# Kernel optimization log

Hardware: AMD Instinct MI355X
Metric: run time of the kernel (lower is better)

## Reference

```python
import jax, jax.numpy as jnp
import numpy as np
from jax import lax

HEADS = 8
DIM_HEAD = 64
MODALITIES = 8
QUERY_DIM = 128
INNER = HEADS * DIM_HEAD  # 512


def _conv(x, w):
    # x: (b, Cin, H, W), w: (Cout, Cin, kh, kw), VALID padding (padding done manually)
    return lax.conv_general_dilated(x, w, window_strides=(1, 1), padding='VALID',
                                    dimension_numbers=('NCHW', 'OIHW', 'NCHW'))


def _reflect_pad_w(x):
    # ReflectionPad2d((2,2,0,0)): pad width (last) axis by 2 on each side
    return jnp.pad(x, ((0, 0), (0, 0), (0, 0), (2, 2)), mode='reflect')


def setup_inputs() -> dict:
    key = jax.random.key(0)
    k1, k2, k3, k4 = jax.random.split(key, 4)
    b, n, m, c = 2, 4096, MODALITIES, QUERY_DIM
    x = jax.random.normal(k1, (b, n, m, c), dtype=jnp.float32)
    Wq = jax.random.normal(k2, (INNER, c, 1, 5), dtype=jnp.float32) * 0.02
    Wkv = jax.random.normal(k3, (2 * INNER, c, 1, 5), dtype=jnp.float32) * 0.02
    Wout = jax.random.normal(k4, (c * m, INNER, m, 5), dtype=jnp.float32) * 0.02
    return {"x": x, "Wq": Wq, "Wkv": Wkv, "Wout": Wout}


def reference(x, Wq, Wkv, Wout):
    b, n, m, c = x.shape
    h, d = HEADS, DIM_HEAD
    scale = d ** -0.5

    xp = _reflect_pad_w(jnp.transpose(x, (0, 3, 2, 1)))  # (b, c, m, n+4)
    q = _conv(xp, Wq)                                     # (b, h*d, m, n)
    kv = _conv(xp, Wkv)                                   # (b, 2*h*d, m, n)
    k, v = kv[:, :h * d], kv[:, h * d:]

    # channel axis (h d) split: h outer, d inner -> (b, h, d, m, n)
    q = q.reshape(b, h, d, m, n)
    k = k.reshape(b, h, d, m, n)
    v = v.reshape(b, h, d, m, n)

    # attention over sequence axis n; feature dim is (m d) per head
    sim = jnp.einsum('bhdmi,bhdmj->bhij', q, k) * scale   # (b, h, n, n)
    attn = jax.nn.softmax(sim, axis=-1)
    out = jnp.einsum('bhij,bhdmj->bhdmi', attn, v)        # (b, h, d, m, n)

    out = out.reshape(b, h * d, m, n)                     # 'b (h d) m n'
    o = _conv(_reflect_pad_w(out), Wout)                  # (b, c*m, 1, n)
    o = o.reshape(b, c, m, 1, n)[:, :, :, 0, :]           # squeeze height-1 dim -> (b, c, m, n)
    return o.reshape(x.shape)                             # torch .view(x_shape) is a raw reshape
```

## Files before the change

### kernel.cpp

```cpp
#include <hip/hip_runtime.h>
#include <stdint.h>


typedef __attribute__((ext_vector_type(8))) short short8;
typedef __attribute__((ext_vector_type(4))) short short4v;
typedef __attribute__((ext_vector_type(2))) short short2v;
typedef __attribute__((ext_vector_type(4))) float f32x4;
typedef __attribute__((ext_vector_type(16))) float f32x16;

__device__ __forceinline__ f32x4 mfma16(short8 a, short8 b, f32x4 c) {
  return __builtin_amdgcn_mfma_f32_16x16x32_bf16(a, b, c, 0, 0, 0);
}
__device__ __forceinline__ f32x16 mfma32(short8 a, short8 b, f32x16 c) {
  return __builtin_amdgcn_mfma_f32_32x32x16_bf16(a, b, c, 0, 0, 0);
}

__device__ __forceinline__ unsigned short f2bf(float f) {
  union { float f; uint32_t u; } v; v.f = f;
  uint32_t r = (v.u + 0x7fffu + ((v.u >> 16) & 1u)) >> 16;
  return (unsigned short)r;
}

__device__ __forceinline__ uint32_t cvtpk(float lo, float hi) {
  uint32_t r;
  asm volatile("v_cvt_pk_bf16_f32 %0, %1, %2" : "=v"(r) : "v"(lo), "v"(hi));
  return r;
}
__device__ __forceinline__ void plswap(uint32_t& a, uint32_t& b) {
  asm volatile("v_permlane32_swap_b32 %0, %1" : "+v"(a), "+v"(b));
}

__device__ __forceinline__ int refl4096(int p) {
  p = p < 0 ? -p : p;
  return p >= 4096 ? 8190 - p : p;
}

__device__ __forceinline__ void gl_lds16(const void* g, void* l) {
  __builtin_amdgcn_global_load_lds(
      (const __attribute__((address_space(1))) void*)g,
      (__attribute__((address_space(3))) void*)l, 16, 0, 0);
}

__global__ void k_convw_qkv(const float* __restrict__ Wq,
                            const float* __restrict__ Wkv,
                            unsigned short* __restrict__ out) {
  int e = blockIdx.x * 256 + threadIdx.x;
  int oc = e / 640, k = e - oc * 640;
  int ci = k & 127, t = k >> 7;
  float w = (oc < 512) ? Wq[oc * 640 + ci * 5 + t]
                       : Wkv[(oc - 512) * 640 + ci * 5 + t];
  out[e] = f2bf(w);
}

__global__ __launch_bounds__(256)
void k_convx(const float* __restrict__ x, unsigned short* __restrict__ xb,
             int b) {
  int e = (blockIdx.x * 256 + threadIdx.x) * 8;
  const float* src = x + (size_t)b * 4194304 + e;
  f32x4 v0 = *(const f32x4*)src;
  f32x4 v1 = *(const f32x4*)(src + 4);
  short8 pk;
  pk[0] = (short)f2bf(v0[0]); pk[1] = (short)f2bf(v0[1]);
  pk[2] = (short)f2bf(v0[2]); pk[3] = (short)f2bf(v0[3]);
  pk[4] = (short)f2bf(v1[0]); pk[5] = (short)f2bf(v1[1]);
  pk[6] = (short)f2bf(v1[2]); pk[7] = (short)f2bf(v1[3]);
  *(short8*)(xb + e) = pk;
}

__global__ __launch_bounds__(256)
void k_convw_out(const float* __restrict__ Wout,
                 unsigned short* __restrict__ out) {
  __shared__ unsigned short row_l[20480];
  const int oc = blockIdx.x;
  const int tid = threadIdx.x;
  const float* src = Wout + (size_t)oc * 20480;
#pragma unroll
  for (int i0 = 0; i0 < 5120; i0 += 256) {
    int i = i0 + tid;
    f32x4 v = *(const f32x4*)(src + (size_t)i * 4);
    short4v pk;
    pk[0] = (short)f2bf(v[0]); pk[1] = (short)f2bf(v[1]);
    pk[2] = (short)f2bf(v[2]); pk[3] = (short)f2bf(v[3]);
    *(short4v*)(row_l + i * 4) = pk;
  }
  __syncthreads();
  unsigned short* drow = out + (size_t)oc * 20480;
#pragma unroll
  for (int r0 = 0; r0 < 20480; r0 += 512) {
    int e = r0 + tid * 2;
    int t0 = e >> 12, ft0 = e & 4095;
    int t1 = (e + 1) >> 12, ft1 = (e + 1) & 4095;
    short2v pk;
    pk[0] = (short)row_l[(ft0 >> 3) * 40 + (ft0 & 7) * 5 + t0];
    pk[1] = (short)row_l[(ft1 >> 3) * 40 + (ft1 & 7) * 5 + t1];
    *(short2v*)(drow + e) = pk;
  }
}

__global__ __launch_bounds__(256)
void k_reduce(const float* __restrict__ P, float* __restrict__ outp, int b) {
  int e = (blockIdx.x * 256 + threadIdx.x) * 4;
  f32x4 a = *(const f32x4*)(P + e);
  f32x4 c = *(const f32x4*)(P + 4194304 + e);
  f32x4 s = (f32x4){a[0] + c[0], a[1] + c[1], a[2] + c[2], a[3] + c[3]};
  *(f32x4*)(outp + (size_t)b * 4194304 + e) = s;
}

__global__ __launch_bounds__(256, 2)
void k_qkv(const unsigned short* __restrict__ xb,
           const unsigned short* __restrict__ Wb,
           unsigned short* __restrict__ Qg, unsigned short* __restrict__ Kg,
           unsigned short* __restrict__ Vg) {
  __shared__ __align__(16) unsigned short As[2][8192];
  __shared__ __align__(16) unsigned short Bs[2][8192];
  const int tid = threadIdx.x;
  const int lane = tid & 63, w = tid >> 6;
  const int wr = w >> 1, wc = w & 1;
  const int l15 = lane & 15, lg = lane >> 4;
  const int p0 = blockIdx.x * 128;
  const int ocb = blockIdx.y * 128;
  const int m = blockIdx.z;

  f32x4 acc[4][4];
#pragma unroll
  for (int i = 0; i < 4; i++)
#pragma unroll
    for (int j = 0; j < 4; j++) acc[i][j] = (f32x4){0.f, 0.f, 0.f, 0.f};

  auto stage = [&](int ks, int d) {
    const int t = ks >> 1;
    const int ci0 = (ks & 1) << 6;
#pragma unroll
    for (int i = 0; i < 4; i++) {
      int s = tid + (i << 8);
      int row = s >> 3, c = s & 7;
      int cs = c ^ (row & 7);
      int xn = refl4096(p0 + row - 2 + t);
      gl_lds16(xb + (((size_t)xn << 3) + m) * 128 + ci0 + (cs << 3),
               (char*)As[d] + (size_t)s * 16);
    }
#pragma unroll
    for (int c = 0; c < 4; c++) {
      int sb = ((c << 2) + w) << 6;
      int slot = sb + lane;
      int row = slot >> 3, cc = slot & 7;
      int cs = cc ^ (row & 7);
      gl_lds16(Wb + (size_t)(ocb + row) * 640 + (ks << 6) + (cs << 3),
               (char*)Bs[d] + (size_t)sb * 16);
    }
  };

  stage(0, 0);

  for (int ks = 0; ks < 10; ks++) {
    const int d = ks & 1;
    __syncthreads();
    if (ks < 9) stage(ks + 1, d ^ 1);
#pragma unroll
    for (int kk = 0; kk < 2; kk++) {
      short8 af[4], bq[4];
#pragma unroll
      for (int i = 0; i < 4; i++) {
        int row = (wr << 6) + (i << 4) + l15;
        af[i] = *(const short8*)((char*)As[d] + (row << 7) +
                                 ((((kk << 2) + lg) ^ (row & 7)) << 4));
      }
#pragma unroll
      for (int j = 0; j < 4; j++) {
        int row = (wc << 6) + (j << 4) + l15;
        bq[j] = *(const short8*)((char*)Bs[d] + (row << 7) +
                                 ((((kk << 2) + lg) ^ (row & 7)) << 4));
      }
#pragma unroll
      for (int i = 0; i < 4; i++)
#pragma unroll
        for (int j = 0; j < 4; j++) acc[i][j] = mfma16(af[i], bq[j], acc[i][j]);
    }
  }

  const int region = ocb >> 9;
  const float QSCALE = 0.18033688f;
#pragma unroll
  for (int i = 0; i < 4; i++) {
    const int posb = p0 + (wr << 6) + (i << 4) + (lg << 2);
#pragma unroll
    for (int j = 0; j < 4; j++) {
      const int oc = ocb + (wc << 6) + (j << 4) + l15;
      const int ocr = oc & 511;
      const int hh = ocr >> 6, dd = ocr & 63;
      const int f = (dd << 3) + m;
      if (region == 0) {
        size_t base = (size_t)hh * 4096 * 512 + f;
#pragma unroll
        for (int r = 0; r < 4; r++)
          Qg[base + (size_t)(posb + r) * 512] = f2bf(acc[i][j][r] * QSCALE);
      } else if (region == 1) {
        size_t base = (size_t)hh * 4096 * 512 + f;
#pragma unroll
        for (int r = 0; r < 4; r++)
          Kg[base + (size_t)(posb + r) * 512] = f2bf(acc[i][j][r]);
      } else {
        short4v pk;
#pragma unroll
        for (int r = 0; r < 4; r++) pk[r] = (short)f2bf(acc[i][j][r]);
        *(short4v*)(Vg + ((size_t)hh * 512 + f) * 4096 + posb) = pk;
      }
    }
  }
}

__global__ __launch_bounds__(512, 2)
void k_attn(const unsigned short* __restrict__ Qg,
            const unsigned short* __restrict__ Kg,
            const unsigned short* __restrict__ Vg,
            unsigned short* __restrict__ AO) {
  __shared__ __align__(16) char lds[131584];
  char* Kt = lds;
  char* Vt0 = lds + 32768;
  char* Vt1 = lds + 65536;
  char* Sx = lds + 98304;
  float* Ls = (float*)(lds + 131072);

  const int tid = threadIdx.x;
  const int lane = tid & 63, w = tid >> 6;
  const int l31 = lane & 31, hi = lane >> 5;
  const int wpair = w >> 1, whalf = w & 1;
  const int h = blockIdx.x & 7;
  const int qblk = blockIdx.x >> 3;
  const int qbase = qblk * 128 + wpair * 32;
  const int fh = whalf << 8;

  const size_t kb = (size_t)h * 4096 * 512;
  const size_t vb = (size_t)h * 512 * 4096;

  short8 q[16];
  {
    const unsigned short* qp =
        Qg + ((size_t)h * 4096 + qbase + l31) * 512 + fh + hi * 8;
#pragma unroll
    for (int ks = 0; ks < 16; ks++) q[ks] = *(const short8*)(qp + ks * 16);
  }

  f32x16 o[8];
#pragma unroll
  for (int t = 0; t < 8; t++)
#pragma unroll
    for (int e = 0; e < 16; e++) o[t][e] = 0.f;
  float lacc = 0.f;

  const int rb = l31 >> 1;
  const int swz = rb & 7;
  const int cg0 = ((l31 & 1) << 2) + hi;
  const int voff1 = rb * 128 + ((cg0 ^ swz) << 4);
  const int voff2 = rb * 128 + (((cg0 + 2) ^ swz) << 4);

  char* sxw = Sx + (w << 10) + (lane << 4);
  char* sxp = Sx + ((w ^ 1) << 10) + (lane << 4);

  union U { uint32_t d[4]; short8 s; };

  auto stageK = [&](int it) {
    const int key0 = it << 5;
#pragma unroll
    for (int i = 0; i < 4; i++) {
      int s = tid + (i << 9);
      int r = s >> 6, c = s & 63;
      gl_lds16(Kg + kb + (size_t)(key0 + r) * 512 + ((c ^ r) << 3),
               Kt + (size_t)s * 16);
    }
  };
  auto stageV = [&](int it, char* Vt) {
    const int key0 = it << 5;
#pragma unroll
    for (int i = 0; i < 4; i++) {
      int s = tid + (i << 9);
      int rp = s >> 3, c = s & 7;
      int cu = c ^ (rp & 7);
      int f = (rp << 1) + (cu >> 2);
      gl_lds16(Vg + vb + (size_t)f * 4096 + key0 + ((cu & 3) << 3),
               Vt + (size_t)s * 16);
    }
  };

  stageK(0);
  stageV(0, Vt0);

  for (int it = 0; it < 128; it++) {
    char* Vt = (it & 1) ? Vt1 : Vt0;
    char* Vn = (it & 1) ? Vt0 : Vt1;
    __syncthreads();

    f32x16 st;
#pragma unroll
    for (int e = 0; e < 16; e++) st[e] = 0.f;
#pragma unroll
    for (int ks = 0; ks < 16; ks++) {
      int ch = ((fh >> 3) + (ks << 1) + hi) ^ l31;
      short8 kfrag = *(const short8*)(Kt + (l31 << 10) + (ch << 4));
      st = mfma32(kfrag, q[ks], st);
    }
#pragma unroll
    for (int j = 0; j < 4; j++) {
      f32x4 pw = (f32x4){st[4 * j], st[4 * j + 1], st[4 * j + 2], st[4 * j + 3]};
      *(f32x4*)(sxw + (j << 13)) = pw;
    }
    __syncthreads();

    if (it < 127) {
      stageK(it + 1);
      stageV(it + 1, Vn);
    }

#pragma unroll
    for (int j = 0; j < 4; j++) {
      f32x4 pv = *(const f32x4*)(sxp + (j << 13));
      st[4 * j] += pv[0]; st[4 * j + 1] += pv[1];
      st[4 * j + 2] += pv[2]; st[4 * j + 3] += pv[3];
    }

    float p[16];
#pragma unroll
    for (int r = 0; r < 16; r++) p[r] = __builtin_amdgcn_exp2f(st[r]);
    lacc += ((p[0] + p[1]) + (p[2] + p[3])) + ((p[4] + p[5]) + (p[6] + p[7])) +
            (((p[8] + p[9]) + (p[10] + p[11])) +
             ((p[12] + p[13]) + (p[14] + p[15])));

    uint32_t d0 = cvtpk(p[0], p[1]),  d1 = cvtpk(p[2], p[3]);
    uint32_t d2 = cvtpk(p[4], p[5]),  d3 = cvtpk(p[6], p[7]);
    uint32_t d4 = cvtpk(p[8], p[9]),  d5 = cvtpk(p[10], p[11]);
    uint32_t d6 = cvtpk(p[12], p[13]), d7 = cvtpk(p[14], p[15]);
    plswap(d0, d2); plswap(d1, d3);
    plswap(d4, d6); plswap(d5, d7);
    U u1; u1.d[0] = d0; u1.d[1] = d1; u1.d[2] = d2; u1.d[3] = d3;
    U u2; u2.d[0] = d4; u2.d[1] = d5; u2.d[2] = d6; u2.d[3] = d7;

#pragma unroll
    for (int tt = 0; tt < 8; tt++) {
      const char* vrow = Vt + (((whalf << 3) + tt) << 11);
      short8 v1 = *(const short8*)(vrow + voff1);
      short8 v2 = *(const short8*)(vrow + voff2);
      o[tt] = mfma32(u1.s, v1, o[tt]);
      o[tt] = mfma32(u2.s, v2, o[tt]);
    }
  }

  lacc += __shfl_xor(lacc, 32, 64);
  if (whalf == 0) Ls[(wpair << 5) + l31] = lacc;
  __syncthreads();

  float linv[16];
#pragma unroll
  for (int r = 0; r < 16; r++) {
    int qq = (r & 3) + ((r >> 2) << 3) + (hi << 2);
    linv[r] = 1.f / Ls[(wpair << 5) + qq];
  }
#pragma unroll
  for (int tt = 0; tt < 8; tt++) {
    size_t col = (size_t)h * 512 + (((whalf << 3) + tt) << 5) + l31;
#pragma unroll
    for (int r = 0; r < 16; r++) {
      int qq = qbase + (r & 3) + ((r >> 2) << 3) + (hi << 2);
      AO[(size_t)qq * 4096 + col] = f2bf(o[tt][r] * linv[r]);
    }
  }
}

__global__ __launch_bounds__(256, 2)
void k_outconv(const unsigned short* __restrict__ AO,
               const unsigned short* __restrict__ WB,
               float* __restrict__ P) {
  __shared__ __align__(16) unsigned short As[2][8192];
  __shared__ __align__(16) unsigned short Bs[2][8192];
  const int tid = threadIdx.x;
  const int lane = tid & 63, w = tid >> 6;
  const int wr = w >> 1, wc = w & 1;
  const int l15 = lane & 15, lg = lane >> 4;
  const int ocb = (blockIdx.x & 7) * 128;
  const int kslice = (blockIdx.x >> 3) & 1;
  const int i0 = (blockIdx.x >> 4) * 128;
  const int ksbase = kslice * 160;

  f32x4 acc[4][4];
#pragma unroll
  for (int i = 0; i < 4; i++)
#pragma unroll
    for (int j = 0; j < 4; j++) acc[i][j] = (f32x4){0.f, 0.f, 0.f, 0.f};

  auto stage = [&](int kabs, int d) {
    const int t = kabs >> 6;
    const int f0 = (kabs & 63) << 6;
    const int k0 = kabs << 6;
#pragma unroll
    for (int i = 0; i < 4; i++) {
      int s = tid + (i << 8);
      int row = s >> 3, c = s & 7;
      int cs = c ^ (row & 7);
      int sr = refl4096(i0 + row + t - 2);
      gl_lds16(AO + (size_t)sr * 4096 + f0 + (cs << 3),
               (char*)As[d] + (size_t)s * 16);
    }
#pragma unroll
    for (int i = 0; i < 4; i++) {
      int s = tid + (i << 8);
      int row = s >> 3, c = s & 7;
      int cs = c ^ (row & 7);
      gl_lds16(WB + (size_t)(ocb + row) * 20480 + k0 + (cs << 3),
               (char*)Bs[d] + (size_t)s * 16);
    }
  };

  stage(ksbase, 0);

  for (int ks = 0; ks < 160; ks++) {
    const int d = ks & 1;
    __syncthreads();
    if (ks < 159) stage(ksbase + ks + 1, d ^ 1);
#pragma unroll
    for (int kk = 0; kk < 2; kk++) {
      short8 af[4], bq[4];
#pragma unroll
      for (int i = 0; i < 4; i++) {
        int row = (wr << 6) + (i << 4) + l15;
        af[i] = *(const short8*)((char*)As[d] + (row << 7) +
                                 ((((kk << 2) + lg) ^ (row & 7)) << 4));
      }
#pragma unroll
      for (int j = 0; j < 4; j++) {
        int row = (wc << 6) + (j << 4) + l15;
        bq[j] = *(const short8*)((char*)Bs[d] + (row << 7) +
                                 ((((kk << 2) + lg) ^ (row & 7)) << 4));
      }
#pragma unroll
      for (int i = 0; i < 4; i++)
#pragma unroll
        for (int j = 0; j < 4; j++) acc[i][j] = mfma16(af[i], bq[j], acc[i][j]);
    }
  }
#pragma unroll
  for (int i = 0; i < 4; i++)
#pragma unroll
    for (int j = 0; j < 4; j++) {
      int oc = ocb + (wc << 6) + (j << 4) + l15;
      int pos = i0 + (wr << 6) + (i << 4) + (lg << 2);
      *(f32x4*)(P + ((size_t)kslice * 1024 + oc) * 4096 + pos) = acc[i][j];
    }
}

extern "C" void kernel_launch(void* const* d_in, const int* in_sizes, int n_in,
                              void* d_out, int out_size, void* d_ws,
                              size_t ws_size, hipStream_t stream) {
  const float* x = (const float*)d_in[0];
  const float* Wq = (const float*)d_in[1];
  const float* Wkv = (const float*)d_in[2];
  const float* Wout = (const float*)d_in[3];
  float* out = (float*)d_out;
  char* ws = (char*)d_ws;

  const size_t SEG = 33554432;
  unsigned short* Qg = (unsigned short*)ws;
  unsigned short* Kg = (unsigned short*)(ws + SEG);
  unsigned short* Vg = (unsigned short*)(ws + 2 * SEG);
  unsigned short* AO = (unsigned short*)(ws + 3 * SEG);
  unsigned short* xb = AO;
  float* Pp = (float*)(ws + 2 * SEG);
  unsigned short* WB1 = (unsigned short*)(ws + 4 * SEG);

  const size_t WB2_OFF = 136183808;
  const size_t WB2_BYTES = (size_t)1024 * 20480 * 2;
  const bool wb2_once = ws_size >= WB2_OFF + WB2_BYTES;
  unsigned short* WB2 =
      wb2_once ? (unsigned short*)(ws + WB2_OFF) : (unsigned short*)ws;

  k_convw_qkv<<<3840, 256, 0, stream>>>(Wq, Wkv, WB1);
  if (wb2_once) k_convw_out<<<1024, 256, 0, stream>>>(Wout, WB2);
  for (int b = 0; b < 2; b++) {
    k_convx<<<2048, 256, 0, stream>>>(x, xb, b);
    k_qkv<<<dim3(32, 12, 8), 256, 0, stream>>>(xb, WB1, Qg, Kg, Vg);
    k_attn<<<256, 512, 0, stream>>>(Qg, Kg, Vg, AO);
    if (!wb2_once) k_convw_out<<<1024, 256, 0, stream>>>(Wout, WB2);
    k_outconv<<<512, 256, 0, stream>>>(AO, WB2, Pp);
    k_reduce<<<4096, 256, 0, stream>>>(Pp, out, b);
  }
}
```

Measured before the change: 1.406 ms.

## Issue V prefetch earlier, raise wave priority around MFMA, hoist address math

```diff
diff --git a/kernel.cpp b/kernel.cpp
--- a/kernel.cpp
+++ b/kernel.cpp
@@ -290,15 +290,19 @@
     char* Vn = (it & 1) ? Vt0 : Vt1;
     __syncthreads();
 
+    if (it < 127) stageV(it + 1, Vn);
+
     f32x16 st;
 #pragma unroll
     for (int e = 0; e < 16; e++) st[e] = 0.f;
+    __builtin_amdgcn_s_setprio(1);
 #pragma unroll
     for (int ks = 0; ks < 16; ks++) {
       int ch = ((fh >> 3) + (ks << 1) + hi) ^ l31;
       short8 kfrag = *(const short8*)(Kt + (l31 << 10) + (ch << 4));
       st = mfma32(kfrag, q[ks], st);
     }
+    __builtin_amdgcn_s_setprio(0);
 #pragma unroll
     for (int j = 0; j < 4; j++) {
       f32x4 pw = (f32x4){st[4 * j], st[4 * j + 1], st[4 * j + 2], st[4 * j + 3]};
@@ -306,10 +310,7 @@
     }
     __syncthreads();
 
-    if (it < 127) {
-      stageK(it + 1);
-      stageV(it + 1, Vn);
-    }
+    if (it < 127) stageK(it + 1);
 
 #pragma unroll
     for (int j = 0; j < 4; j++) {
@@ -334,6 +335,7 @@
     U u1; u1.d[0] = d0; u1.d[1] = d1; u1.d[2] = d2; u1.d[3] = d3;
     U u2; u2.d[0] = d4; u2.d[1] = d5; u2.d[2] = d6; u2.d[3] = d7;
 
+    __builtin_amdgcn_s_setprio(1);
 #pragma unroll
     for (int tt = 0; tt < 8; tt++) {
       const char* vrow = Vt + (((whalf << 3) + tt) << 11);
@@ -342,6 +344,7 @@
       o[tt] = mfma32(u1.s, v1, o[tt]);
       o[tt] = mfma32(u2.s, v2, o[tt]);
     }
+    __builtin_amdgcn_s_setprio(0);
   }
 
   lacc += __shfl_xor(lacc, 32, 64);
@@ -386,26 +389,50 @@
 #pragma unroll
     for (int j = 0; j < 4; j++) acc[i][j] = (f32x4){0.f, 0.f, 0.f, 0.f};
 
+  size_t bbase[4];
+#pragma unroll
+  for (int i = 0; i < 4; i++) {
+    int s = tid + (i << 8);
+    int row = s >> 3, c = s & 7;
+    int cs = c ^ (row & 7);
+    bbase[i] = (size_t)(ocb + row) * 20480 + (cs << 3);
+  }
+
+  size_t aoff[4];
+  uint32_t bk = 0;
+  bool first = true;
+
   auto stage = [&](int kabs, int d) {
-    const int t = kabs >> 6;
-    const int f0 = (kabs & 63) << 6;
-    const int k0 = kabs << 6;
+    if (first) {
+      bk = (uint32_t)kabs << 6;
+    } else {
+      bk += 64;
+    }
+    if (first || (kabs & 63) == 0) {
+      const int t = kabs >> 6;
+      const int f0 = (kabs & 63) << 6;
+#pragma unroll
+      for (int i = 0; i < 4; i++) {
+        int s = tid + (i << 8);
+        int row = s >> 3, c = s & 7;
+        int cs = c ^ (row & 7);
+        int sr = refl4096(i0 + row + t - 2);
+        aoff[i] = (size_t)sr * 4096 + f0 + (cs << 3);
+      }
+      first = false;
+    } else {
+#pragma unroll
+      for (int i = 0; i < 4; i++) aoff[i] += 64;
+    }
 #pragma unroll
     for (int i = 0; i < 4; i++) {
       int s = tid + (i << 8);
-      int row = s >> 3, c = s & 7;
-      int cs = c ^ (row & 7);
-      int sr = refl4096(i0 + row + t - 2);
-      gl_lds16(AO + (size_t)sr * 4096 + f0 + (cs << 3),
-               (char*)As[d] + (size_t)s * 16);
+      gl_lds16(AO + aoff[i], (char*)As[d] + (size_t)s * 16);
     }
 #pragma unroll
     for (int i = 0; i < 4; i++) {
       int s = tid + (i << 8);
-      int row = s >> 3, c = s & 7;
-      int cs = c ^ (row & 7);
-      gl_lds16(WB + (size_t)(ocb + row) * 20480 + k0 + (cs << 3),
-               (char*)Bs[d] + (size_t)s * 16);
+      gl_lds16(WB + bbase[i] + bk, (char*)Bs[d] + (size_t)s * 16);
     }
   };
 
@@ -415,6 +442,7 @@
     const int d = ks & 1;
     __syncthreads();
     if (ks < 159) stage(ksbase + ks + 1, d ^ 1);
+    __builtin_amdgcn_s_setprio(1);
 #pragma unroll
     for (int kk = 0; kk < 2; kk++) {
       short8 af[4], bq[4];
@@ -435,6 +463,7 @@
 #pragma unroll
         for (int j = 0; j < 4; j++) acc[i][j] = mfma16(af[i], bq[j], acc[i][j]);
     }
+    __builtin_amdgcn_s_setprio(0);
   }
 #pragma unroll
   for (int i = 0; i < 4; i++)
```

Result: faster. 1.325 ms, median of 2 (-5.7%).
